# Kernel tuning notes

Measured on AMD Instinct MI355X. Metric: run time of the kernel, lower is better.

The kernel has to match this reference:

```python
import jax, jax.numpy as jnp
import numpy as np

N, E, D, C, M = 50000, 600000, 128, 40, 25000


def setup_inputs() -> dict:
    key = jax.random.key(0)
    ks = jax.random.split(key, 10)
    s = 1.0 / np.sqrt(D)
    return {
        "x": jax.random.normal(ks[0], (N, D), jnp.float32),
        "edge_index": jax.random.randint(ks[1], (2, E), 0, N, jnp.int64),
        "node_label_index": jax.random.randint(ks[2], (M,), 0, N, jnp.int64),
        "W0": jax.random.normal(ks[3], (D, D), jnp.float32) * s,
        "b0": jnp.zeros((D,), jnp.float32),
        "W1": jax.random.normal(ks[4], (D, D), jnp.float32) * s,
        "b1": jnp.zeros((D,), jnp.float32),
        "W2": jax.random.normal(ks[5], (D, D), jnp.float32) * s,
        "b2": jnp.zeros((D,), jnp.float32),
        "W3": jax.random.normal(ks[6], (D, D), jnp.float32) * s,
        "b3": jnp.zeros((D,), jnp.float32),
        "Wh": jax.random.normal(ks[7], (D, C), jnp.float32) * s,
        "bh": jnp.zeros((C,), jnp.float32),
    }


def _gcn(x, W, b, src, dst, dinv):
    h = x @ W                                    # [N, D']
    norm = (dinv[src] * dinv[dst])[:, None]      # [E, 1]
    agg = jax.ops.segment_sum(h[src] * norm, dst, num_segments=x.shape[0])
    return agg + h * (dinv ** 2)[:, None] + b    # self-loop term + bias


def reference(x, edge_index, node_label_index, W0, b0, W1, b1, W2, b2, W3, b3, Wh, bh):
    src, dst = edge_index[0], edge_index[1]
    # degree with self-loops (PyG counts in-degree on dst after add_self_loops)
    deg = 1.0 + jax.ops.segment_sum(jnp.ones((src.shape[0],), x.dtype), dst,
                                    num_segments=x.shape[0])
    dinv = jax.lax.rsqrt(deg)

    cell0 = _gcn(x, W0, b0, src, dst, dinv)
    cell1 = _gcn(jax.nn.relu(cell0), W1, b1, src, dst, dinv)
    cell2 = (_gcn(jax.nn.relu(cell0), W2, b2, src, dst, dinv)
             + _gcn(jax.nn.relu(cell1), W2, b2, src, dst, dinv))
    cell3 = (_gcn(jax.nn.relu(cell0), W3, b3, src, dst, dinv)
             + _gcn(jax.nn.relu(cell1), W3, b3, src, dst, dinv)
             + _gcn(jax.nn.relu(cell2), W3, b3, src, dst, dinv))

    feat = jax.nn.log_softmax(cell3, axis=1)
    pred = (feat @ Wh + bh)[node_label_index]    # [M, C]
    return pred
```

## Files before the change

### kernel.cpp

```cpp
#include <hip/hip_runtime.h>
#include <hip/hip_bf16.h>
#include <cstdint>
#include <cstddef>

#define DIM 128

typedef __attribute__((ext_vector_type(8))) short bf16x8;
typedef __attribute__((ext_vector_type(4))) float f32x4;

__device__ __forceinline__ unsigned short f2bf(float f) {
    __hip_bfloat16 h = __float2bfloat16(f);
    return *(unsigned short*)&h;
}
__device__ __forceinline__ unsigned pack_bf2(float a, float b) {
    return (unsigned)f2bf(a) | ((unsigned)f2bf(b) << 16);
}
__device__ __forceinline__ float bflo(unsigned u) { return __uint_as_float(u << 16); }
__device__ __forceinline__ float bfhi(unsigned u) { return __uint_as_float(u & 0xffff0000u); }

union U4B8 { uint4 q; bf16x8 v; };

__global__ __launch_bounds__(256)
void k_init(const int* __restrict__ dst, int* __restrict__ count,
            int* __restrict__ rank, int e, int egrid,
            const float* __restrict__ W0, const float* __restrict__ W1,
            const float* __restrict__ W2, const float* __restrict__ W3,
            const float* __restrict__ Wh,
            unsigned short* __restrict__ Wpk,
            unsigned short* __restrict__ WhP,
            float* __restrict__ whs,
            unsigned short* __restrict__ H, int n, int C) {
    if ((int)blockIdx.x < egrid) {
        int i = blockIdx.x * 256 + threadIdx.x;
        if (i < e) rank[i] = atomicAdd(&count[dst[i]], 1);
        return;
    }
    const int NW = 4 * DIM * DIM;
    const int NH = 3 * 4 * 64 * 8;
    int g = (blockIdx.x - egrid) * 256 + threadIdx.x;
    if (g < NW) {
        int j   = g & 7;
        int ln  = (g >> 3) & 63;
        int kc  = (g >> 9) & 3;
        int nt  = (g >> 11) & 7;
        int mat = g >> 14;
        const float* W = (mat == 0) ? W0 : (mat == 1) ? W1 : (mat == 2) ? W2 : W3;
        int k = kc * 32 + (ln >> 4) * 8 + j;
        int nc = nt * 16 + (ln & 15);
        Wpk[g] = f2bf(W[k * DIM + nc]);
    } else if (g < NW + NH) {
        int gg = g - NW;
        int j  = gg & 7;
        int ln = (gg >> 3) & 63;
        int kc = (gg >> 9) & 3;
        int nt = gg >> 11;
        int k  = kc * 32 + (ln >> 4) * 8 + j;
        int nc = nt * 16 + (ln & 15);
        WhP[gg] = (nc < C) ? f2bf(Wh[k * C + nc]) : (unsigned short)0;
    } else if (g < NW + NH + 64) {
        int c = g - NW - NH;
        if (c < C) {
            float s = 0.f;
            for (int d = 0; d < DIM; ++d) s += Wh[d * C + c];
            whs[c] = s;
        }
    } else if (g < NW + NH + 64 + 16) {
        int t = g - (NW + NH + 64);
        uint4 z; z.x = z.y = z.z = z.w = 0u;
        ((uint4*)H)[(size_t)n * 16 + t] = z;
    }
}

__global__ __launch_bounds__(1024)
void k_scanA(const int* __restrict__ count, int* __restrict__ partial,
             int* __restrict__ bsum, float* __restrict__ dinv, int n) {
    __shared__ int wsum[16];
    int tid = threadIdx.x, lane = tid & 63, wid = tid >> 6;
    int i = blockIdx.x * 1024 + tid;
    int v = (i < n) ? count[i] : 0;
    if (i < n) dinv[i] = rsqrtf(1.0f + (float)v);
    int x = v;
    #pragma unroll
    for (int off = 1; off < 64; off <<= 1) {
        int y = __shfl_up(x, off, 64);
        if (lane >= off) x += y;
    }
    if (lane == 63) wsum[wid] = x;
    __syncthreads();
    int waveoff = 0, total = 0;
    #pragma unroll
    for (int w = 0; w < 16; ++w) {
        int s = wsum[w];
        if (w < wid) waveoff += s;
        total += s;
    }
    if (i < n) partial[i] = x + waveoff;
    if (tid == 0) bsum[blockIdx.x] = total;
}

__global__ __launch_bounds__(1024)
void k_scanB(const int* __restrict__ partial, const int* __restrict__ bsum,
             int* __restrict__ row_ptr, int n, int nb) {
    __shared__ int s_off;
    int tid = threadIdx.x;
    if (tid < 64) {
        int carry = 0;
        for (int base = 0; base < nb; base += 64) {
            int idx = base + tid;
            int v = (idx < nb && idx < blockIdx.x) ? bsum[idx] : 0;
            #pragma unroll
            for (int off = 32; off > 0; off >>= 1) v += __shfl_xor(v, off, 64);
            carry += v;
        }
        if (tid == 0) s_off = carry;
    }
    __syncthreads();
    int off = s_off;
    int i = blockIdx.x * 1024 + tid;
    if (i < n) row_ptr[i + 1] = partial[i] + off;
    if (blockIdx.x == 0 && tid == 0) row_ptr[0] = 0;
}

__global__ __launch_bounds__(256)
void k_fillmm(const float* __restrict__ in, const unsigned short* __restrict__ Wpk,
              const float* __restrict__ dinv, unsigned short* __restrict__ outp, int n,
              const int* __restrict__ src, const int* __restrict__ dst,
              const int* __restrict__ rank, const int* __restrict__ row_ptr,
              int* __restrict__ colv, int e, int mmg) {
    if ((int)blockIdx.x >= mmg) {
        int i = (blockIdx.x - mmg) * 256 + threadIdx.x;
        if (i < e) {
            int d = dst[i];
            int r = rank[i];
            colv[row_ptr[d] + r] = src[i];
        }
        return;
    }
    int wv   = threadIdx.x >> 6;
    int lane = threadIdx.x & 63;
    int r0   = blockIdx.x * 64 + wv * 16;
    int m    = lane & 15;
    int quad = lane >> 4;

    bf16x8 afr[4];
    int arow = r0 + m;
    bool rowok = arow < n;
    const float* ap = in + (size_t)arow * DIM + quad * 8;
    #pragma unroll
    for (int kc = 0; kc < 4; ++kc) {
        float4 p0, p1;
        if (rowok) {
            p0 = *(const float4*)(ap + kc * 32);
            p1 = *(const float4*)(ap + kc * 32 + 4);
        } else {
            p0.x = p0.y = p0.z = p0.w = 0.f;
            p1.x = p1.y = p1.z = p1.w = 0.f;
        }
        union { bf16x8 v; unsigned short u[8]; } a;
        a.u[0] = f2bf(p0.x); a.u[1] = f2bf(p0.y);
        a.u[2] = f2bf(p0.z); a.u[3] = f2bf(p0.w);
        a.u[4] = f2bf(p1.x); a.u[5] = f2bf(p1.y);
        a.u[6] = f2bf(p1.z); a.u[7] = f2bf(p1.w);
        afr[kc] = a.v;
    }

    float dsc[4];
    #pragma unroll
    for (int t = 0; t < 4; ++t) {
        int r = r0 + quad * 4 + t;
        dsc[t] = (r < n) ? dinv[r] : 0.f;
    }

    const uint4* wp = (const uint4*)Wpk;
    #pragma unroll
    for (int nt = 0; nt < 8; ++nt) {
        f32x4 acc = {0.f, 0.f, 0.f, 0.f};
        #pragma unroll
        for (int kc = 0; kc < 4; ++kc) {
            U4B8 b; b.q = wp[(nt * 4 + kc) * 64 + lane];
            acc = __builtin_amdgcn_mfma_f32_16x16x32_bf16(afr[kc], b.v, acc, 0, 0, 0);
        }
        int colb = nt * 16 + m;
        #pragma unroll
        for (int t = 0; t < 4; ++t) {
            int r = r0 + quad * 4 + t;
            if (r < n)
                outp[(size_t)r * DIM + colb] = f2bf(dsc[t] * acc[t]);
        }
    }
}

__global__ __launch_bounds__(256)
void k_matmul_b(const unsigned short* __restrict__ in, const unsigned short* __restrict__ Wpk,
                const float* __restrict__ dinv, unsigned short* __restrict__ outp, int n) {
    int wv   = threadIdx.x >> 6;
    int lane = threadIdx.x & 63;
    int r0   = blockIdx.x * 64 + wv * 16;
    int m    = lane & 15;
    int quad = lane >> 4;

    bf16x8 afr[4];
    int arow = r0 + m;
    bool rowok = arow < n;
    const uint4* in16 = (const uint4*)in;
    #pragma unroll
    for (int kc = 0; kc < 4; ++kc) {
        U4B8 a;
        if (rowok) a.q = in16[(size_t)arow * 16 + kc * 4 + quad];
        else { a.q.x = a.q.y = a.q.z = a.q.w = 0u; }
        afr[kc] = a.v;
    }

    float dsc[4];
    #pragma unroll
    for (int t = 0; t < 4; ++t) {
        int r = r0 + quad * 4 + t;
        dsc[t] = (r < n) ? dinv[r] : 0.f;
    }

    const uint4* wp = (const uint4*)Wpk;
    #pragma unroll
    for (int nt = 0; nt < 8; ++nt) {
        f32x4 acc = {0.f, 0.f, 0.f, 0.f};
        #pragma unroll
        for (int kc = 0; kc < 4; ++kc) {
            U4B8 b; b.q = wp[(nt * 4 + kc) * 64 + lane];
            acc = __builtin_amdgcn_mfma_f32_16x16x32_bf16(afr[kc], b.v, acc, 0, 0, 0);
        }
        int colb = nt * 16 + m;
        #pragma unroll
        for (int t = 0; t < 4; ++t) {
            int r = r0 + quad * 4 + t;
            if (r < n)
                outp[(size_t)r * DIM + colb] = f2bf(dsc[t] * acc[t]);
        }
    }
}

__global__ __launch_bounds__(256)
void k_prop(const unsigned short* __restrict__ h, const int* __restrict__ row_ptr,
            const int* __restrict__ col, const float* __restrict__ dinv,
            const float* __restrict__ bias, float bscale,
            const unsigned short* addin, unsigned short* __restrict__ outp, int n) {
    int node = (blockIdx.x * 256 + threadIdx.x) >> 6;
    int lane = threadIdx.x & 63;
    if (node >= n) return;
    int beg = row_ptr[node], end = row_ptr[node + 1];
    float di = dinv[node];
    int qid = lane >> 4;
    int fo  = lane & 15;
    const uint4* h16 = (const uint4*)h;
    uint4 sd = h16[((unsigned)node << 4) | fo];
    float aL0 = 0.f, aH0 = 0.f, aL1 = 0.f, aH1 = 0.f;
    float aL2 = 0.f, aH2 = 0.f, aL3 = 0.f, aH3 = 0.f;
    float bL0 = 0.f, bH0 = 0.f, bL1 = 0.f, bH1 = 0.f;
    float bL2 = 0.f, bH2 = 0.f, bL3 = 0.f, bH3 = 0.f;
    int j = beg + qid;
    int s0 = (j < end) ? col[j] : n;
    int s1 = (j + 4 < end) ? col[j + 4] : n;
    while (s0 != n) {
        uint4 d0 = h16[((unsigned)s0 << 4) | fo];
        uint4 d1 = h16[((unsigned)s1 << 4) | fo];
        int jn = j + 8;
        s0 = (jn < end) ? col[jn] : n;
        s1 = (jn + 4 < end) ? col[jn + 4] : n;
        j = jn;
        aL0 += bflo(d0.x); aH0 += bfhi(d0.x);
        aL1 += bflo(d0.y); aH1 += bfhi(d0.y);
        aL2 += bflo(d0.z); aH2 += bfhi(d0.z);
        aL3 += bflo(d0.w); aH3 += bfhi(d0.w);
        bL0 += bflo(d1.x); bH0 += bfhi(d1.x);
        bL1 += bflo(d1.y); bH1 += bfhi(d1.y);
        bL2 += bflo(d1.z); bH2 += bfhi(d1.z);
        bL3 += bflo(d1.w); bH3 += bfhi(d1.w);
    }
    uint4 av; av.x = av.y = av.z = av.w = 0u;
    if (addin) av = ((const uint4*)addin)[(size_t)node * 16 + fo];
    aL0 += bL0; aH0 += bH0; aL1 += bL1; aH1 += bH1;
    aL2 += bL2; aH2 += bH2; aL3 += bL3; aH3 += bH3;
    aL0 += __shfl_xor(aL0, 16, 64); aL0 += __shfl_xor(aL0, 32, 64);
    aH0 += __shfl_xor(aH0, 16, 64); aH0 += __shfl_xor(aH0, 32, 64);
    aL1 += __shfl_xor(aL1, 16, 64); aL1 += __shfl_xor(aL1, 32, 64);
    aH1 += __shfl_xor(aH1, 16, 64); aH1 += __shfl_xor(aH1, 32, 64);
    aL2 += __shfl_xor(aL2, 16, 64); aL2 += __shfl_xor(aL2, 32, 64);
    aH2 += __shfl_xor(aH2, 16, 64); aH2 += __shfl_xor(aH2, 32, 64);
    aL3 += __shfl_xor(aL3, 16, 64); aL3 += __shfl_xor(aL3, 32, 64);
    aH3 += __shfl_xor(aH3, 16, 64); aH3 += __shfl_xor(aH3, 32, 64);
    aL0 += bflo(sd.x); aH0 += bfhi(sd.x);
    aL1 += bflo(sd.y); aH1 += bfhi(sd.y);
    aL2 += bflo(sd.z); aH2 += bfhi(sd.z);
    aL3 += bflo(sd.w); aH3 += bfhi(sd.w);
    if (lane < 16) {
        const float4* b4 = (const float4*)bias;
        float4 bA = b4[2 * fo], bB = b4[2 * fo + 1];
        float r0x = fmaxf(fmaf(bscale, bA.x, di * aL0), 0.f);
        float r0y = fmaxf(fmaf(bscale, bA.y, di * aH0), 0.f);
        float r0z = fmaxf(fmaf(bscale, bA.z, di * aL1), 0.f);
        float r0w = fmaxf(fmaf(bscale, bA.w, di * aH1), 0.f);
        float r1x = fmaxf(fmaf(bscale, bB.x, di * aL2), 0.f);
        float r1y = fmaxf(fmaf(bscale, bB.y, di * aH2), 0.f);
        float r1z = fmaxf(fmaf(bscale, bB.z, di * aL3), 0.f);
        float r1w = fmaxf(fmaf(bscale, bB.w, di * aH3), 0.f);
        r0x += bflo(av.x); r0y += bfhi(av.x);
        r0z += bflo(av.y); r0w += bfhi(av.y);
        r1x += bflo(av.z); r1y += bfhi(av.z);
        r1z += bflo(av.w); r1w += bfhi(av.w);
        size_t base = (size_t)node * 16 + fo;
        uint4 o;
        o.x = pack_bf2(r0x, r0y);
        o.y = pack_bf2(r0z, r0w);
        o.z = pack_bf2(r1x, r1y);
        o.w = pack_bf2(r1z, r1w);
        ((uint4*)outp)[base] = o;
    }
}

__global__ __launch_bounds__(1024)
void k_propv_head(const unsigned short* __restrict__ h, const int* __restrict__ row_ptr,
                  const int* __restrict__ col, const float* __restrict__ dinv,
                  const float* __restrict__ bias, float bscale,
                  const int* __restrict__ labels,
                  const unsigned short* __restrict__ WhP, const float* __restrict__ whs,
                  const float* __restrict__ bh, float* __restrict__ outp,
                  int m_total, int C, int n) {
    __shared__ uint4 Vs[16 * 17];
    __shared__ float Ls[16];
    int wid  = threadIdx.x >> 6;
    int lane = threadIdx.x & 63;
    int m = blockIdx.x * 16 + wid;
    bool valid = m < m_total;
    int node = valid ? labels[m] : 0;
    int beg = 0, end = 0;
    if (valid) { beg = row_ptr[node]; end = row_ptr[node + 1]; }
    float di = dinv[node];
    int qid = lane >> 4, fo = lane & 15;
    const uint4* h16 = (const uint4*)h;
    uint4 sd = h16[((unsigned)node << 4) | fo];
    float aL0 = 0.f, aH0 = 0.f, aL1 = 0.f, aH1 = 0.f;
    float aL2 = 0.f, aH2 = 0.f, aL3 = 0.f, aH3 = 0.f;
    float bL0 = 0.f, bH0 = 0.f, bL1 = 0.f, bH1 = 0.f;
    float bL2 = 0.f, bH2 = 0.f, bL3 = 0.f, bH3 = 0.f;
    int j = beg + qid;
    int s0 = (j < end) ? col[j] : n;
    int s1 = (j + 4 < end) ? col[j + 4] : n;
    while (s0 != n) {
        uint4 d0 = h16[((unsigned)s0 << 4) | fo];
        uint4 d1 = h16[((unsigned)s1 << 4) | fo];
        int jn = j + 8;
        s0 = (jn < end) ? col[jn] : n;
        s1 = (jn + 4 < end) ? col[jn + 4] : n;
        j = jn;
        aL0 += bflo(d0.x); aH0 += bfhi(d0.x);
        aL1 += bflo(d0.y); aH1 += bfhi(d0.y);
        aL2 += bflo(d0.z); aH2 += bfhi(d0.z);
        aL3 += bflo(d0.w); aH3 += bfhi(d0.w);
        bL0 += bflo(d1.x); bH0 += bfhi(d1.x);
        bL1 += bflo(d1.y); bH1 += bfhi(d1.y);
        bL2 += bflo(d1.z); bH2 += bfhi(d1.z);
        bL3 += bflo(d1.w); bH3 += bfhi(d1.w);
    }
    aL0 += bL0; aH0 += bH0; aL1 += bL1; aH1 += bH1;
    aL2 += bL2; aH2 += bH2; aL3 += bL3; aH3 += bH3;
    aL0 += __shfl_xor(aL0, 16, 64); aL0 += __shfl_xor(aL0, 32, 64);
    aH0 += __shfl_xor(aH0, 16, 64); aH0 += __shfl_xor(aH0, 32, 64);
    aL1 += __shfl_xor(aL1, 16, 64); aL1 += __shfl_xor(aL1, 32, 64);
    aH1 += __shfl_xor(aH1, 16, 64); aH1 += __shfl_xor(aH1, 32, 64);
    aL2 += __shfl_xor(aL2, 16, 64); aL2 += __shfl_xor(aL2, 32, 64);
    aH2 += __shfl_xor(aH2, 16, 64); aH2 += __shfl_xor(aH2, 32, 64);
    aL3 += __shfl_xor(aL3, 16, 64); aL3 += __shfl_xor(aL3, 32, 64);
    aH3 += __shfl_xor(aH3, 16, 64); aH3 += __shfl_xor(aH3, 32, 64);
    aL0 += bflo(sd.x); aH0 += bfhi(sd.x);
    aL1 += bflo(sd.y); aH1 += bfhi(sd.y);
    aL2 += bflo(sd.z); aH2 += bfhi(sd.z);
    aL3 += bflo(sd.w); aH3 += bfhi(sd.w);
    const float4* b4 = (const float4*)bias;
    float4 bA = b4[2 * fo], bB = b4[2 * fo + 1];
    float v0 = fmaf(bscale, bA.x, di * aL0);
    float v1 = fmaf(bscale, bA.y, di * aH0);
    float v2 = fmaf(bscale, bA.z, di * aL1);
    float v3 = fmaf(bscale, bA.w, di * aH1);
    float v4 = fmaf(bscale, bB.x, di * aL2);
    float v5 = fmaf(bscale, bB.y, di * aH2);
    float v6 = fmaf(bscale, bB.z, di * aL3);
    float v7 = fmaf(bscale, bB.w, di * aH3);
    float mx = fmaxf(fmaxf(fmaxf(v0, v1), fmaxf(v2, v3)),
                     fmaxf(fmaxf(v4, v5), fmaxf(v6, v7)));
    #pragma unroll
    for (int off = 8; off > 0; off >>= 1) mx = fmaxf(mx, __shfl_xor(mx, off, 64));
    float se = expf(v0 - mx) + expf(v1 - mx) + expf(v2 - mx) + expf(v3 - mx)
             + expf(v4 - mx) + expf(v5 - mx) + expf(v6 - mx) + expf(v7 - mx);
    #pragma unroll
    for (int off = 8; off > 0; off >>= 1) se += __shfl_xor(se, off, 64);
    float L = mx + logf(se);
    if (lane < 16) {
        uint4 o;
        o.x = pack_bf2(v0, v1);
        o.y = pack_bf2(v2, v3);
        o.z = pack_bf2(v4, v5);
        o.w = pack_bf2(v6, v7);
        Vs[wid * 17 + fo] = o;
    }
    if (lane == 0) Ls[wid] = L;
    __syncthreads();
    if (wid < 3) {
        int mm = lane & 15, quad = lane >> 4;
        bf16x8 afr[4];
        #pragma unroll
        for (int kc = 0; kc < 4; ++kc) {
            U4B8 a; a.q = Vs[mm * 17 + kc * 4 + quad];
            afr[kc] = a.v;
        }
        float lv[4];
        #pragma unroll
        for (int t = 0; t < 4; ++t) lv[t] = Ls[quad * 4 + t];
        const uint4* wp = (const uint4*)WhP;
        f32x4 acc = {0.f, 0.f, 0.f, 0.f};
        #pragma unroll
        for (int kc = 0; kc < 4; ++kc) {
            U4B8 b; b.q = wp[(wid * 4 + kc) * 64 + lane];
            acc = __builtin_amdgcn_mfma_f32_16x16x32_bf16(afr[kc], b.v, acc, 0, 0, 0);
        }
        int colc = wid * 16 + mm;
        if (colc < C) {
            float wsc = whs[colc], bc = bh[colc];
            #pragma unroll
            for (int t = 0; t < 4; ++t) {
                int r = blockIdx.x * 16 + quad * 4 + t;
                if (r < m_total)
                    outp[(size_t)r * C + colc] = acc[t] - lv[t] * wsc + bc;
            }
        }
    }
}

extern "C" void kernel_launch(void* const* d_in, const int* in_sizes, int n_in,
                              void* d_out, int out_size, void* d_ws, size_t ws_size,
                              hipStream_t stream) {
    const float* x      = (const float*)d_in[0];
    const int*   edges  = (const int*)d_in[1];
    const int*   labels = (const int*)d_in[2];
    const float* W0 = (const float*)d_in[3];
    const float* b0 = (const float*)d_in[4];
    const float* W1 = (const float*)d_in[5];
    const float* b1 = (const float*)d_in[6];
    const float* W2 = (const float*)d_in[7];
    const float* b2 = (const float*)d_in[8];
    const float* W3 = (const float*)d_in[9];
    const float* b3 = (const float*)d_in[10];
    const float* Wh = (const float*)d_in[11];
    const float* bh = (const float*)d_in[12];
    float* out = (float*)d_out;

    const int N = in_sizes[0] / DIM;
    const int E = in_sizes[1] / 2;
    const int M = in_sizes[2];
    const int C = in_sizes[12];

    char* ws = (char*)d_ws;
    auto alloc = [&](size_t bytes) {
        char* p = ws;
        ws += (bytes + 255) & ~(size_t)255;
        return p;
    };
    float* dinv    = (float*)alloc((size_t)N * 4);
    int*   count   = (int*)  alloc((size_t)N * 4);
    int*   row_ptr = (int*)  alloc((size_t)(N + 1) * 4);
    int*   rank    = (int*)  alloc((size_t)E * 4);
    int*   partial = (int*)  alloc((size_t)N * 4);
    int*   bsum    = (int*)  alloc(64 * 4);
    int*   col     = (int*)  alloc((size_t)E * 4);
    float* whs     = (float*)alloc(256);
    unsigned short* Wpk = (unsigned short*)alloc((size_t)4 * DIM * DIM * 2);
    unsigned short* WhP = (unsigned short*)alloc((size_t)3 * 4 * 64 * 8 * 2);
    unsigned short* H   = (unsigned short*)alloc((size_t)(N + 1) * DIM * 2);
    unsigned short* R0  = (unsigned short*)alloc((size_t)N * DIM * 2);
    unsigned short* A   = (unsigned short*)alloc((size_t)N * DIM * 2);

    const int* src = edges;
    const int* dst = edges + E;

    int egrid  = (E + 255) / 256;
    int sgrid  = (N + 1023) / 1024;
    int mmgrid = (N + 63) / 64;
    int pgrid  = (N + 3) / 4;
    const int FR = DIM * DIM;
    const int NPACK = 4 * FR + 3 * 4 * 64 * 8 + 64 + 16;
    int packgrid = (NPACK + 255) / 256;

    hipMemsetAsync(count, 0, (size_t)N * 4, stream);
    k_init <<<egrid + packgrid, 256, 0, stream>>>(dst, count, rank, E, egrid,
                                                  W0, W1, W2, W3, Wh,
                                                  Wpk, WhP, whs, H, N, C);
    k_scanA<<<sgrid, 1024, 0, stream>>>(count, partial, bsum, dinv, N);
    k_scanB<<<sgrid, 1024, 0, stream>>>(partial, bsum, row_ptr, N, sgrid);
    k_fillmm<<<mmgrid + egrid, 256, 0, stream>>>(x, Wpk, dinv, H, N,
                                                 src, dst, rank, row_ptr, col, E, mmgrid);
    k_prop    <<<pgrid, 256, 0, stream>>>(H, row_ptr, col, dinv, b0, 1.f, nullptr, R0, N);
    k_matmul_b<<<mmgrid, 256, 0, stream>>>(R0, Wpk + 1 * FR, dinv, H, N);
    k_prop    <<<pgrid, 256, 0, stream>>>(H, row_ptr, col, dinv, b1, 1.f, R0, A, N);
    k_matmul_b<<<mmgrid, 256, 0, stream>>>(A, Wpk + 2 * FR, dinv, H, N);
    k_prop    <<<pgrid, 256, 0, stream>>>(H, row_ptr, col, dinv, b2, 2.f, A, A, N);
    k_matmul_b<<<mmgrid, 256, 0, stream>>>(A, Wpk + 3 * FR, dinv, H, N);
    k_propv_head<<<(M + 15) / 16, 1024, 0, stream>>>(H, row_ptr, col, dinv, b3, 3.f,
                                                     labels, WhP, whs, bh, out, M, C, N);
}
```

Baseline: 286.3 us.

## Reorder last layer to aggregate before matmul and fold W3 into head weights

The final full-graph matmul over all N nodes is removed. The last layer now aggregates the input features (scaled by dinv per neighbor) only for the M label nodes, then multiplies by W3 inside the head kernel to compute log_softmax. The head uses a precomputed W3·Wh combined weight and a combined bias. This trades an N-row matmul for extra per-edge dinv gathers and more MFMA work and shared-memory reductions per block, plus a serial 128-term dot per element of the precomputed combined weights.

```diff
diff --git a/kernel.cpp b/kernel.cpp
--- a/kernel.cpp
+++ b/kernel.cpp
@@ -25,11 +25,13 @@
             int* __restrict__ rank, int e, int egrid,
             const float* __restrict__ W0, const float* __restrict__ W1,
             const float* __restrict__ W2, const float* __restrict__ W3,
-            const float* __restrict__ Wh,
+            const float* __restrict__ Wh, const float* __restrict__ b3,
+            const float* __restrict__ bh,
             unsigned short* __restrict__ Wpk,
-            unsigned short* __restrict__ WhP,
-            float* __restrict__ whs,
-            unsigned short* __restrict__ H, int n, int C) {
+            unsigned short* __restrict__ WcombP,
+            float* __restrict__ whs, float* __restrict__ bcomb,
+            unsigned short* __restrict__ H, unsigned short* __restrict__ Abuf,
+            float* __restrict__ dinv, int n, int C) {
     if ((int)blockIdx.x < egrid) {
         int i = blockIdx.x * 256 + threadIdx.x;
         if (i < e) rank[i] = atomicAdd(&count[dst[i]], 1);
@@ -56,18 +58,33 @@
         int nt = gg >> 11;
         int k  = kc * 32 + (ln >> 4) * 8 + j;
         int nc = nt * 16 + (ln & 15);
-        WhP[gg] = (nc < C) ? f2bf(Wh[k * C + nc]) : (unsigned short)0;
+        float s = 0.f;
+        if (nc < C) {
+            for (int d = 0; d < DIM; ++d) s += W3[k * DIM + d] * Wh[d * C + nc];
+        }
+        WcombP[gg] = f2bf(s);
     } else if (g < NW + NH + 64) {
         int c = g - NW - NH;
         if (c < C) {
-            float s = 0.f;
-            for (int d = 0; d < DIM; ++d) s += Wh[d * C + c];
-            whs[c] = s;
+            float s = 0.f, t = 0.f;
+            for (int d = 0; d < DIM; ++d) {
+                float w = Wh[d * C + c];
+                s += w;
+                t += b3[d] * w;
+            }
+            whs[c]   = s;
+            bcomb[c] = 3.0f * t + bh[c];
         }
     } else if (g < NW + NH + 64 + 16) {
         int t = g - (NW + NH + 64);
         uint4 z; z.x = z.y = z.z = z.w = 0u;
         ((uint4*)H)[(size_t)n * 16 + t] = z;
+    } else if (g < NW + NH + 64 + 32) {
+        int t = g - (NW + NH + 64 + 16);
+        uint4 z; z.x = z.y = z.z = z.w = 0u;
+        ((uint4*)Abuf)[(size_t)n * 16 + t] = z;
+    } else if (g == NW + NH + 64 + 32) {
+        dinv[n] = 0.f;
     }
 }
 
@@ -316,14 +333,18 @@
 }
 
 __global__ __launch_bounds__(1024)
-void k_propv_head(const unsigned short* __restrict__ h, const int* __restrict__ row_ptr,
-                  const int* __restrict__ col, const float* __restrict__ dinv,
-                  const float* __restrict__ bias, float bscale,
-                  const int* __restrict__ labels,
-                  const unsigned short* __restrict__ WhP, const float* __restrict__ whs,
-                  const float* __restrict__ bh, float* __restrict__ outp,
-                  int m_total, int C, int n) {
+void k_propv_fused(const unsigned short* __restrict__ A, const int* __restrict__ row_ptr,
+                   const int* __restrict__ col, const float* __restrict__ dinv,
+                   const float* __restrict__ b3, float bscale,
+                   const int* __restrict__ labels,
+                   const unsigned short* __restrict__ W3pk,
+                   const unsigned short* __restrict__ WcombP,
+                   const float* __restrict__ whs, const float* __restrict__ bcomb,
+                   float* __restrict__ outp, int m_total, int C, int n) {
     __shared__ uint4 Vs[16 * 17];
+    __shared__ float Ds[16];
+    __shared__ float Mred[8 * 16];
+    __shared__ float Sred[8 * 16];
     __shared__ float Ls[16];
     int wid  = threadIdx.x >> 6;
     int lane = threadIdx.x & 63;
@@ -334,7 +355,7 @@
     if (valid) { beg = row_ptr[node]; end = row_ptr[node + 1]; }
     float di = dinv[node];
     int qid = lane >> 4, fo = lane & 15;
-    const uint4* h16 = (const uint4*)h;
+    const uint4* h16 = (const uint4*)A;
     uint4 sd = h16[((unsigned)node << 4) | fo];
     float aL0 = 0.f, aH0 = 0.f, aL1 = 0.f, aH1 = 0.f;
     float aL2 = 0.f, aH2 = 0.f, aL3 = 0.f, aH3 = 0.f;
@@ -343,21 +364,24 @@
     int j = beg + qid;
     int s0 = (j < end) ? col[j] : n;
     int s1 = (j + 4 < end) ? col[j + 4] : n;
+    float w0 = dinv[s0], w1 = dinv[s1];
     while (s0 != n) {
         uint4 d0 = h16[((unsigned)s0 << 4) | fo];
         uint4 d1 = h16[((unsigned)s1 << 4) | fo];
+        float cw0 = w0, cw1 = w1;
         int jn = j + 8;
         s0 = (jn < end) ? col[jn] : n;
         s1 = (jn + 4 < end) ? col[jn + 4] : n;
+        w0 = dinv[s0]; w1 = dinv[s1];
         j = jn;
-        aL0 += bflo(d0.x); aH0 += bfhi(d0.x);
-        aL1 += bflo(d0.y); aH1 += bfhi(d0.y);
-        aL2 += bflo(d0.z); aH2 += bfhi(d0.z);
-        aL3 += bflo(d0.w); aH3 += bfhi(d0.w);
-        bL0 += bflo(d1.x); bH0 += bfhi(d1.x);
-        bL1 += bflo(d1.y); bH1 += bfhi(d1.y);
-        bL2 += bflo(d1.z); bH2 += bfhi(d1.z);
-        bL3 += bflo(d1.w); bH3 += bfhi(d1.w);
+        aL0 = fmaf(cw0, bflo(d0.x), aL0); aH0 = fmaf(cw0, bfhi(d0.x), aH0);
+        aL1 = fmaf(cw0, bflo(d0.y), aL1); aH1 = fmaf(cw0, bfhi(d0.y), aH1);
+        aL2 = fmaf(cw0, bflo(d0.z), aL2); aH2 = fmaf(cw0, bfhi(d0.z), aH2);
+        aL3 = fmaf(cw0, bflo(d0.w), aL3); aH3 = fmaf(cw0, bfhi(d0.w), aH3);
+        bL0 = fmaf(cw1, bflo(d1.x), bL0); bH0 = fmaf(cw1, bfhi(d1.x), bH0);
+        bL1 = fmaf(cw1, bflo(d1.y), bL1); bH1 = fmaf(cw1, bfhi(d1.y), bH1);
+        bL2 = fmaf(cw1, bflo(d1.z), bL2); bH2 = fmaf(cw1, bfhi(d1.z), bH2);
+        bL3 = fmaf(cw1, bflo(d1.w), bL3); bH3 = fmaf(cw1, bfhi(d1.w), bH3);
     }
     aL0 += bL0; aH0 += bH0; aL1 += bL1; aH1 += bH1;
     aL2 += bL2; aH2 += bH2; aL3 += bL3; aH3 += bH3;
@@ -369,65 +393,109 @@
     aH2 += __shfl_xor(aH2, 16, 64); aH2 += __shfl_xor(aH2, 32, 64);
     aL3 += __shfl_xor(aL3, 16, 64); aL3 += __shfl_xor(aL3, 32, 64);
     aH3 += __shfl_xor(aH3, 16, 64); aH3 += __shfl_xor(aH3, 32, 64);
-    aL0 += bflo(sd.x); aH0 += bfhi(sd.x);
-    aL1 += bflo(sd.y); aH1 += bfhi(sd.y);
-    aL2 += bflo(sd.z); aH2 += bfhi(sd.z);
-    aL3 += bflo(sd.w); aH3 += bfhi(sd.w);
-    const float4* b4 = (const float4*)bias;
-    float4 bA = b4[2 * fo], bB = b4[2 * fo + 1];
-    float v0 = fmaf(bscale, bA.x, di * aL0);
-    float v1 = fmaf(bscale, bA.y, di * aH0);
-    float v2 = fmaf(bscale, bA.z, di * aL1);
-    float v3 = fmaf(bscale, bA.w, di * aH1);
-    float v4 = fmaf(bscale, bB.x, di * aL2);
-    float v5 = fmaf(bscale, bB.y, di * aH2);
-    float v6 = fmaf(bscale, bB.z, di * aL3);
-    float v7 = fmaf(bscale, bB.w, di * aH3);
-    float mx = fmaxf(fmaxf(fmaxf(v0, v1), fmaxf(v2, v3)),
-                     fmaxf(fmaxf(v4, v5), fmaxf(v6, v7)));
-    #pragma unroll
-    for (int off = 8; off > 0; off >>= 1) mx = fmaxf(mx, __shfl_xor(mx, off, 64));
-    float se = expf(v0 - mx) + expf(v1 - mx) + expf(v2 - mx) + expf(v3 - mx)
-             + expf(v4 - mx) + expf(v5 - mx) + expf(v6 - mx) + expf(v7 - mx);
-    #pragma unroll
-    for (int off = 8; off > 0; off >>= 1) se += __shfl_xor(se, off, 64);
-    float L = mx + logf(se);
+    aL0 = fmaf(di, bflo(sd.x), aL0); aH0 = fmaf(di, bfhi(sd.x), aH0);
+    aL1 = fmaf(di, bflo(sd.y), aL1); aH1 = fmaf(di, bfhi(sd.y), aH1);
+    aL2 = fmaf(di, bflo(sd.z), aL2); aH2 = fmaf(di, bfhi(sd.z), aH2);
+    aL3 = fmaf(di, bflo(sd.w), aL3); aH3 = fmaf(di, bfhi(sd.w), aH3);
     if (lane < 16) {
         uint4 o;
-        o.x = pack_bf2(v0, v1);
-        o.y = pack_bf2(v2, v3);
-        o.z = pack_bf2(v4, v5);
-        o.w = pack_bf2(v6, v7);
+        o.x = pack_bf2(aL0, aH0);
+        o.y = pack_bf2(aL1, aH1);
+        o.z = pack_bf2(aL2, aH2);
+        o.w = pack_bf2(aL3, aH3);
         Vs[wid * 17 + fo] = o;
     }
-    if (lane == 0) Ls[wid] = L;
+    if (lane == 0) Ds[wid] = di;
     __syncthreads();
-    if (wid < 3) {
-        int mm = lane & 15, quad = lane >> 4;
+
+    f32x4 hacc = {0.f, 0.f, 0.f, 0.f};
+    float cell[4] = {0.f, 0.f, 0.f, 0.f};
+    float gmx[4]  = {0.f, 0.f, 0.f, 0.f};
+    int mm = lane & 15, quad = lane >> 4;
+    if (wid < 8) {
+        int nt = wid;
         bf16x8 afr[4];
         #pragma unroll
         for (int kc = 0; kc < 4; ++kc) {
             U4B8 a; a.q = Vs[mm * 17 + kc * 4 + quad];
             afr[kc] = a.v;
         }
-        float lv[4];
-        #pragma unroll
-        for (int t = 0; t < 4; ++t) lv[t] = Ls[quad * 4 + t];
-        const uint4* wp = (const uint4*)WhP;
         f32x4 acc = {0.f, 0.f, 0.f, 0.f};
+        const uint4* wp = (const uint4*)W3pk;
         #pragma unroll
         for (int kc = 0; kc < 4; ++kc) {
-            U4B8 b; b.q = wp[(wid * 4 + kc) * 64 + lane];
+            U4B8 b; b.q = wp[(nt * 4 + kc) * 64 + lane];
             acc = __builtin_amdgcn_mfma_f32_16x16x32_bf16(afr[kc], b.v, acc, 0, 0, 0);
         }
-        int colc = wid * 16 + mm;
+        float b3c = bscale * b3[nt * 16 + mm];
+        #pragma unroll
+        for (int t = 0; t < 4; ++t) {
+            int row = quad * 4 + t;
+            cell[t] = fmaf(Ds[row], acc[t], b3c);
+            float mxv = cell[t];
+            #pragma unroll
+            for (int off = 1; off < 16; off <<= 1)
+                mxv = fmaxf(mxv, __shfl_xor(mxv, off, 64));
+            if (mm == 0) Mred[nt * 16 + row] = mxv;
+        }
+    } else if (wid < 11) {
+        int nth = wid - 8;
+        bf16x8 afr[4];
+        #pragma unroll
+        for (int kc = 0; kc < 4; ++kc) {
+            U4B8 a; a.q = Vs[mm * 17 + kc * 4 + quad];
+            afr[kc] = a.v;
+        }
+        const uint4* wp = (const uint4*)WcombP;
+        #pragma unroll
+        for (int kc = 0; kc < 4; ++kc) {
+            U4B8 b; b.q = wp[(nth * 4 + kc) * 64 + lane];
+            hacc = __builtin_amdgcn_mfma_f32_16x16x32_bf16(afr[kc], b.v, hacc, 0, 0, 0);
+        }
+    }
+    __syncthreads();
+
+    if (wid < 8) {
+        int nt = wid;
+        #pragma unroll
+        for (int t = 0; t < 4; ++t) {
+            int row = quad * 4 + t;
+            float g = Mred[row];
+            #pragma unroll
+            for (int i = 1; i < 8; ++i) g = fmaxf(g, Mred[i * 16 + row]);
+            gmx[t] = g;
+            float e = expf(cell[t] - g);
+            #pragma unroll
+            for (int off = 1; off < 16; off <<= 1) e += __shfl_xor(e, off, 64);
+            if (mm == 0) Sred[nt * 16 + row] = e;
+        }
+    }
+    __syncthreads();
+
+    if (wid == 0 && mm == 0) {
+        #pragma unroll
+        for (int t = 0; t < 4; ++t) {
+            int row = quad * 4 + t;
+            float s = Sred[row];
+            #pragma unroll
+            for (int i = 1; i < 8; ++i) s += Sred[i * 16 + row];
+            Ls[row] = gmx[t] + logf(s);
+        }
+    }
+    __syncthreads();
+
+    if (wid >= 8 && wid < 11) {
+        int nth = wid - 8;
+        int colc = nth * 16 + mm;
         if (colc < C) {
-            float wsc = whs[colc], bc = bh[colc];
+            float wsc = whs[colc], bc = bcomb[colc];
             #pragma unroll
             for (int t = 0; t < 4; ++t) {
-                int r = blockIdx.x * 16 + quad * 4 + t;
+                int row = quad * 4 + t;
+                int r = blockIdx.x * 16 + row;
                 if (r < m_total)
-                    outp[(size_t)r * C + colc] = acc[t] - lv[t] * wsc + bc;
+                    outp[(size_t)r * C + colc] =
+                        fmaf(Ds[row], hacc[t], bc) - Ls[row] * wsc;
             }
         }
     }
@@ -462,7 +530,7 @@
         ws += (bytes + 255) & ~(size_t)255;
         return p;
     };
-    float* dinv    = (float*)alloc((size_t)N * 4);
+    float* dinv    = (float*)alloc((size_t)(N + 1) * 4);
     int*   count   = (int*)  alloc((size_t)N * 4);
     int*   row_ptr = (int*)  alloc((size_t)(N + 1) * 4);
     int*   rank    = (int*)  alloc((size_t)E * 4);
@@ -470,11 +538,12 @@
     int*   bsum    = (int*)  alloc(64 * 4);
     int*   col     = (int*)  alloc((size_t)E * 4);
     float* whs     = (float*)alloc(256);
-    unsigned short* Wpk = (unsigned short*)alloc((size_t)4 * DIM * DIM * 2);
-    unsigned short* WhP = (unsigned short*)alloc((size_t)3 * 4 * 64 * 8 * 2);
+    float* bcomb   = (float*)alloc(256);
+    unsigned short* Wpk    = (unsigned short*)alloc((size_t)4 * DIM * DIM * 2);
+    unsigned short* WcombP = (unsigned short*)alloc((size_t)3 * 4 * 64 * 8 * 2);
     unsigned short* H   = (unsigned short*)alloc((size_t)(N + 1) * DIM * 2);
     unsigned short* R0  = (unsigned short*)alloc((size_t)N * DIM * 2);
-    unsigned short* A   = (unsigned short*)alloc((size_t)N * DIM * 2);
+    unsigned short* A   = (unsigned short*)alloc((size_t)(N + 1) * DIM * 2);
 
     const int* src = edges;
     const int* dst = edges + E;
@@ -484,13 +553,14 @@
     int mmgrid = (N + 63) / 64;
     int pgrid  = (N + 3) / 4;
     const int FR = DIM * DIM;
-    const int NPACK = 4 * FR + 3 * 4 * 64 * 8 + 64 + 16;
+    const int NPACK = 4 * FR + 3 * 4 * 64 * 8 + 64 + 33;
     int packgrid = (NPACK + 255) / 256;
 
     hipMemsetAsync(count, 0, (size_t)N * 4, stream);
     k_init <<<egrid + packgrid, 256, 0, stream>>>(dst, count, rank, E, egrid,
-                                                  W0, W1, W2, W3, Wh,
-                                                  Wpk, WhP, whs, H, N, C);
+                                                  W0, W1, W2, W3, Wh, b3, bh,
+                                                  Wpk, WcombP, whs, bcomb,
+                                                  H, A, dinv, N, C);
     k_scanA<<<sgrid, 1024, 0, stream>>>(count, partial, bsum, dinv, N);
     k_scanB<<<sgrid, 1024, 0, stream>>>(partial, bsum, row_ptr, N, sgrid);
     k_fillmm<<<mmgrid + egrid, 256, 0, stream>>>(x, Wpk, dinv, H, N,
@@ -500,7 +570,7 @@
     k_prop    <<<pgrid, 256, 0, stream>>>(H, row_ptr, col, dinv, b1, 1.f, R0, A, N);
     k_matmul_b<<<mmgrid, 256, 0, stream>>>(A, Wpk + 2 * FR, dinv, H, N);
     k_prop    <<<pgrid, 256, 0, stream>>>(H, row_ptr, col, dinv, b2, 2.f, A, A, N);
-    k_matmul_b<<<mmgrid, 256, 0, stream>>>(A, Wpk + 3 * FR, dinv, H, N);
-    k_propv_head<<<(M + 15) / 16, 1024, 0, stream>>>(H, row_ptr, col, dinv, b3, 3.f,
-                                                     labels, WhP, whs, bh, out, M, C, N);
-}
+    k_propv_fused<<<(M + 15) / 16, 1024, 0, stream>>>(A, row_ptr, col, dinv, b3, 3.f,
+                                                      labels, Wpk + 3 * FR, WcombP,
+                                                      whs, bcomb, out, M, C, N);
+}
```

Measured after the change: 282.0 us. About the same (-1.5%).
